# Optimization experiments

Hardware: AMD Instinct MI355X
Metric: run time of the kernel (lower is better)

Reference implementation:

```python
import jax, jax.numpy as jnp
import numpy as np

LAMBDA_MIN = 0.1
LAMBDA_GLOBAL_MIN = 0.1
LAMBDA_GLOBAL_SCALE = 1.0
SLOPE = 0.2  # negative_slope


def leaky(x):
    return jnp.where(x >= 0, x, SLOPE * x)


def setup_inputs() -> dict:
    key = jax.random.key(0)
    ks = jax.random.split(key, 16)
    n, d, E, C, R = 10000, 128, 320000, 50000, 20
    s = 0.05
    h = jax.random.normal(ks[0], (n, d), jnp.float32)
    edge_index = jax.random.randint(ks[1], (2, E), 0, n)
    edge_type = jax.random.randint(ks[2], (E,), 0, R)
    rel_table = jax.random.normal(ks[3], (R, d), jnp.float32) * s
    # constraints taken from a subset of edges so matches exist
    constraint_indices = edge_index[:, :C]
    constraint_values = jax.random.normal(ks[4], (C,), jnp.float32)
    constraint_types = jax.random.randint(ks[5], (C,), 0, 4)
    att_in = 3 * d  # out*2 + in_dim (use_relation)
    W = jax.random.normal(ks[6], (d, d), jnp.float32) * s
    W_bi = jax.random.normal(ks[7], (d, d), jnp.float32) * s
    att_w1 = jax.random.normal(ks[8], (d, att_in), jnp.float32) * s
    att_b1 = jnp.zeros((d,), jnp.float32)
    att_w2 = jax.random.normal(ks[9], (d,), jnp.float32) * s
    gate_w1 = jax.random.normal(ks[10], (d, 2 * d), jnp.float32) * s
    gate_b1 = jnp.zeros((d,), jnp.float32)
    gate_w2 = jax.random.normal(ks[11], (d,), jnp.float32) * s
    gate_b2 = jnp.zeros((), jnp.float32)
    lambda_c = jnp.full((4,), 0.5, jnp.float32)  # CONSTRAINT_LAMBDA_INIT
    lambda_global = jnp.array(0.5, jnp.float32)
    return dict(h=h, edge_index=edge_index, edge_type=edge_type,
                rel_table=rel_table, constraint_indices=constraint_indices,
                constraint_values=constraint_values, constraint_types=constraint_types,
                W=W, W_bi=W_bi, att_w1=att_w1, att_b1=att_b1, att_w2=att_w2,
                gate_w1=gate_w1, gate_b1=gate_b1, gate_w2=gate_w2, gate_b2=gate_b2,
                lambda_c=lambda_c, lambda_global=lambda_global)


def reference(h, edge_index, edge_type, rel_table, constraint_indices,
              constraint_values, constraint_types, W, W_bi, att_w1, att_b1,
              att_w2, gate_w1, gate_b1, gate_w2, gate_b2, lambda_c, lambda_global):
    n = h.shape[0]
    Wh = h @ W.T                                  # [n, d]
    src, tgt = edge_index[0], edge_index[1]
    src_emb, tgt_emb = Wh[src], Wh[tgt]           # [E, d]
    r_emb = rel_table[edge_type]                  # [E, d]
    att_in = jnp.concatenate([src_emb, tgt_emb, r_emb], axis=-1)  # [E, 3d]
    e = leaky(att_in @ att_w1.T + att_b1) @ att_w2                # [E]

    # ---- constraints (bounded lambdas) ----
    lc = jax.nn.sigmoid(lambda_c) * (1.0 - LAMBDA_MIN) + LAMBDA_MIN
    lg = jax.nn.sigmoid(lambda_global) * (LAMBDA_GLOBAL_SCALE - LAMBDA_GLOBAL_MIN) + LAMBDA_GLOBAL_MIN
    ws = lc[constraint_types] * constraint_values                 # [C]
    c_keys = constraint_indices[0] * n + constraint_indices[1]
    e_keys = src * n + tgt
    # O(n^2) scatter buffers, faithful to the original
    c_agg = jnp.zeros((n * n,), jnp.float32).at[c_keys].add(ws)
    c_exists = jnp.zeros((n * n,), jnp.float32).at[c_keys].add(1.0)
    ms = c_agg[e_keys]
    mask = c_exists[e_keys] > 0
    ms = ms * mask.astype(jnp.float32)
    # constraint gate on matched edges (unmatched entries are 0 anyway)
    gi = jnp.concatenate([src_emb, tgt_emb], axis=-1)             # [E, 2d]
    g = jax.nn.sigmoid(leaky(gi @ gate_w1.T + gate_b1) @ gate_w2 + gate_b2)
    ms = jnp.where(mask, g * ms, ms)
    n_matched = mask.sum()
    global_bias = lg * jnp.mean(ws) * 0.01
    e = jnp.where(n_matched > 0, e + lg * ms, e + global_bias)

    # ---- scatter softmax over src neighborhoods ----
    mx = jax.ops.segment_max(e, src, num_segments=n)
    ex = jnp.exp(jnp.minimum(e - mx[src], 20.0))
    sm = jax.ops.segment_sum(ex, src, num_segments=n)
    attn = ex / (sm[src] + 1e-10)                                 # [E]

    # ---- weighted scatter-add aggregation ----
    side = jax.ops.segment_sum(attn[:, None] * tgt_emb, src, num_segments=n)  # [n, d]

    sum_out = leaky(Wh + side)
    bi_out = leaky((Wh * side) @ W_bi.T)
    h_new = sum_out + bi_out + Wh   # bi-interaction + residual
    return jax.nn.elu(h_new)
```

## Files before the change

### kernel.cpp

```cpp
#include <hip/hip_runtime.h>
#include <stdint.h>

#define SLOPE 0.2f
#define HASH_SIZE 131072
#define POIS ((int)0xAAAAAAAA)
#define MAXDEG 64

typedef __attribute__((ext_vector_type(8))) short bf16x8;
typedef __attribute__((ext_vector_type(4))) float f32x4;

__device__ __forceinline__ float leakyf(float x) { return fmaxf(x, SLOPE * x); }
__device__ __forceinline__ float sigmoidf(float x) { return 1.f / (1.f + __expf(-x)); }
__device__ __forceinline__ unsigned short f2bf(float f) {
  union { float f; unsigned int i; } c; c.f = f;
  unsigned int u = c.i;
  return (unsigned short)((u + 0x7fffu + ((u >> 16) & 1u)) >> 16);
}
__device__ __forceinline__ void unpk8(uint4 v, float* o) {
  union { unsigned int i; float f; } t;
  t.i = v.x << 16;          o[0] = t.f;
  t.i = v.x & 0xffff0000u;  o[1] = t.f;
  t.i = v.y << 16;          o[2] = t.f;
  t.i = v.y & 0xffff0000u;  o[3] = t.f;
  t.i = v.z << 16;          o[4] = t.f;
  t.i = v.z & 0xffff0000u;  o[5] = t.f;
  t.i = v.w << 16;          o[6] = t.f;
  t.i = v.w & 0xffff0000u;  o[7] = t.f;
}
__device__ __forceinline__ void ldbf8(const unsigned short* p, float* o) {
  unpk8(*(const uint4*)p, o);
}

__device__ __forceinline__ void mfma_core_a(const bf16x8 (&afr)[4],
                                            const unsigned short* bptr, f32x4 (&acc)[8]) {
  #pragma unroll
  for (int ks = 0; ks < 4; ++ks) {
    #pragma unroll
    for (int ct = 0; ct < 8; ++ct) {
      bf16x8 b = *(const bf16x8*)(bptr + ct * 2048 + ks * 32);
      acc[ct] = __builtin_amdgcn_mfma_f32_16x16x32_bf16(afr[ks], b, acc[ct], 0, 0, 0);
    }
  }
}

__global__ __launch_bounds__(256) void setup_kernel(
    const float* __restrict__ aw1, const float* __restrict__ gw1,
    const float* __restrict__ W, const float* __restrict__ Wbi,
    const float* __restrict__ rel, const float* __restrict__ ab1,
    const int* __restrict__ cidx, const float* __restrict__ cval,
    const int* __restrict__ ctype, const float* __restrict__ lc,
    unsigned short* __restrict__ Wcat, unsigned short* __restrict__ P3b16,
    int* __restrict__ hkeys,
    int C, int n, int R, int H)
{
  int i0 = blockIdx.x * blockDim.x + threadIdx.x;
  int stride = gridDim.x * blockDim.x;
  for (int j = i0; j < 6 * 16384; j += stride) {
    int mat = j >> 14, rest = j & 16383, col = rest >> 7, k = rest & 127;
    float v;
    switch (mat) {
      case 0:  v = aw1[col * 384 + k]; break;
      case 1:  v = aw1[col * 384 + 128 + k]; break;
      case 2:  v = gw1[col * 256 + k]; break;
      case 3:  v = gw1[col * 256 + 128 + k]; break;
      case 4:  v = W[col * 128 + k]; break;
      default: v = Wbi[col * 128 + k]; break;
    }
    Wcat[j] = f2bf(v);
  }
  for (int it = i0; it < R * 128; it += stride) {
    int r = it >> 7, jj = it & 127;
    float acc = ab1[jj];
    const float4* wrow = (const float4*)(aw1 + jj * 384 + 256);
    const float4* rl   = (const float4*)(rel + r * 128);
    #pragma unroll 8
    for (int k = 0; k < 32; ++k) {
      float4 a = rl[k], b = wrow[k];
      acc += a.x * b.x + a.y * b.y + a.z * b.z + a.w * b.w;
    }
    P3b16[it] = f2bf(acc);
  }
  for (int j = i0; j < C; j += stride) {
    int key = cidx[j] * n + cidx[C + j];
    float l = sigmoidf(lc[ctype[j]]) * 0.9f + 0.1f;
    float w = l * cval[j];
    unsigned int slot = ((unsigned int)key * 2654435761u) & (unsigned int)(H - 1);
    while (true) {
      int prev = atomicCAS(&hkeys[2 * slot], POIS, key);
      if (prev == POIS || prev == key) break;
      slot = (slot + 1) & (unsigned int)(H - 1);
    }
    atomicAdd((float*)&hkeys[2 * slot + 1], w);
  }
}

__device__ __forceinline__ void store_tile(const unsigned short (*t)[136],
                                           unsigned short* __restrict__ out,
                                           int rs, int rows_left, int lane)
{
  const int c = (lane & 15) * 8, q = lane >> 4;
  #pragma unroll
  for (int ro = 0; ro < 4; ++ro) {
    int row = ro * 4 + q;
    bf16x8 v = *(const bf16x8*)&t[row][c];
    if (row < rows_left)
      *(bf16x8*)(out + row * rs + c) = v;
  }
}

__global__ __launch_bounds__(256) void gemm_place(
    const int* __restrict__ ei, const int* __restrict__ etype,
    int* __restrict__ cursor2, int2* __restrict__ trs2, int E,
    const float* __restrict__ h, const unsigned short* __restrict__ Wcat,
    const int2* __restrict__ hk,
    unsigned short* __restrict__ PW, unsigned short* __restrict__ PQ,
    unsigned short* __restrict__ Q2b,
    int n, int NB5, int H)
{
  if ((int)blockIdx.x >= NB5) {
    int i = ((int)blockIdx.x - NB5) * 256 + threadIdx.x;
    if (i < E) {
      int s = ei[i], t = ei[E + i], rt = etype[i];
      float ms = 0.f;
      bool found = false;
      int key = s * n + t;
      unsigned int slot = ((unsigned int)key * 2654435761u) & (unsigned int)(H - 1);
      while (true) {
        int2 kv = hk[slot];
        if (kv.x == key) { ms = __int_as_float(kv.y); found = true; break; }
        if (kv.x == POIS) break;
        slot = (slot + 1) & (unsigned int)(H - 1);
      }
      int rec = t | (rt << 14);
      if (found) {
        int k = atomicAdd(&cursor2[2 * s], 1) - POIS;
        if (k < MAXDEG)
          trs2[(size_t)s * MAXDEG + k] = make_int2(rec, __float_as_int(ms));
      } else {
        int k = atomicAdd(&cursor2[2 * s + 1], 1) - POIS;
        int bp = MAXDEG - 1 - k;
        if (bp >= 0)
          trs2[(size_t)s * MAXDEG + bp] = make_int2(rec, 0);
      }
    }
    return;
  }
  __shared__ unsigned short tile[4][16][136];
  const int wv = (int)threadIdx.x >> 6, lane = (int)threadIdx.x & 63;
  const int m0 = ((int)blockIdx.x * 4 + wv) * 16;
  if (m0 >= n) return;
  const int r = lane & 15, quad = lane >> 4;
  const int rows_left = n - m0;

  bf16x8 afr[4];
  const float* hrow = h + (size_t)min(m0 + r, n - 1) * 128 + quad * 8;
  #pragma unroll
  for (int ks = 0; ks < 4; ++ks) {
    float4 f0 = *(const float4*)(hrow + ks * 32);
    float4 f1 = *(const float4*)(hrow + ks * 32 + 4);
    bf16x8 a;
    a[0] = (short)f2bf(f0.x); a[1] = (short)f2bf(f0.y);
    a[2] = (short)f2bf(f0.z); a[3] = (short)f2bf(f0.w);
    a[4] = (short)f2bf(f1.x); a[5] = (short)f2bf(f1.y);
    a[6] = (short)f2bf(f1.z); a[7] = (short)f2bf(f1.w);
    afr[ks] = a;
  }

  f32x4 acc[8] = {};
  mfma_core_a(afr, Wcat + 4 * 16384 + r * 128 + quad * 8, acc);
  #pragma unroll
  for (int ct = 0; ct < 8; ++ct)
    #pragma unroll
    for (int rg = 0; rg < 4; ++rg)
      tile[wv][quad * 4 + rg][ct * 16 + r] = f2bf(acc[ct][rg]);

  bf16x8 wfr[4];
  #pragma unroll
  for (int ks = 0; ks < 4; ++ks)
    wfr[ks] = *(const bf16x8*)&tile[wv][r][quad * 8 + ks * 32];

  store_tile(tile[wv], PW + (size_t)m0 * 256 + 128, 256, rows_left, lane);

  #pragma unroll
  for (int mat = 0; mat < 4; ++mat) {
    f32x4 a2[8] = {};
    mfma_core_a(wfr, Wcat + mat * 16384 + r * 128 + quad * 8, a2);
    #pragma unroll
    for (int ct = 0; ct < 8; ++ct)
      #pragma unroll
      for (int rg = 0; rg < 4; ++rg)
        tile[wv][quad * 4 + rg][ct * 16 + r] = f2bf(a2[ct][rg]);
    unsigned short* out; int rs;
    if (mat == 0)      { out = PQ  + (size_t)m0 * 256;        rs = 256; }
    else if (mat == 1) { out = PW  + (size_t)m0 * 256;        rs = 256; }
    else if (mat == 2) { out = PQ  + (size_t)m0 * 256 + 128;  rs = 256; }
    else               { out = Q2b + (size_t)m0 * 128;        rs = 128; }
    store_tile(tile[wv], out, rs, rows_left, lane);
  }
}

__global__ __launch_bounds__(256) void fused_node_final(
  const int* __restrict__ cursor2,
  const int2* __restrict__ trs2,
  const unsigned short* __restrict__ PQ, const unsigned short* __restrict__ PW,
  const unsigned short* __restrict__ P3b16, const unsigned short* __restrict__ Q2,
  const float* __restrict__ aw2, const float* __restrict__ gb1,
  const float* __restrict__ gw2, const float* __restrict__ gb2,
  const float* __restrict__ lgp,
  const unsigned short* __restrict__ Wcat5,
  float* __restrict__ outp, int n, int R)
{
  __shared__ unsigned short P3l[20 * 128];
  __shared__ unsigned short Xt[4][136];
  __shared__ float          Ft[4][132];

  for (int j = threadIdx.x; j < R * 64; j += 256)
    ((unsigned int*)P3l)[j] = ((const unsigned int*)P3b16)[j];
  __syncthreads();

  const int wv = (int)threadIdx.x >> 6;
  const int lane = (int)threadIdx.x & 63;
  const int g = lane >> 4;
  const int u = lane & 15;
  const int d0 = u * 8;

  const int node = (int)blockIdx.x * 4 + wv;
  const bool anode = node < n;

  if (anode) {
    const int2 cc2 = *(const int2*)&cursor2[2 * node];
    const int cM = min(cc2.x - POIS, MAXDEG);
    const int cU = min(cc2.y - POIS, MAXDEG - cM);
    const int2 ment = trs2[(size_t)node * MAXDEG + lane];

    float p1v[8], w2v[8], qbv[8], g2v[8];
    const unsigned short* pqrow = PQ + (size_t)node * 256 + d0;
    ldbf8(pqrow, p1v);
    { float q1t[8]; ldbf8(pqrow + 128, q1t);
      float4 bA = *(const float4*)(gb1 + d0), bB = *(const float4*)(gb1 + d0 + 4);
      qbv[0]=q1t[0]+bA.x; qbv[1]=q1t[1]+bA.y; qbv[2]=q1t[2]+bA.z; qbv[3]=q1t[3]+bA.w;
      qbv[4]=q1t[4]+bB.x; qbv[5]=q1t[5]+bB.y; qbv[6]=q1t[6]+bB.z; qbv[7]=q1t[7]+bB.w; }
    { float4 a = *(const float4*)(aw2 + d0), b = *(const float4*)(aw2 + d0 + 4);
      w2v[0]=a.x; w2v[1]=a.y; w2v[2]=a.z; w2v[3]=a.w;
      w2v[4]=b.x; w2v[5]=b.y; w2v[6]=b.z; w2v[7]=b.w; }
    { float4 a = *(const float4*)(gw2 + d0), b = *(const float4*)(gw2 + d0 + 4);
      g2v[0]=a.x; g2v[1]=a.y; g2v[2]=a.z; g2v[3]=a.w;
      g2v[4]=b.x; g2v[5]=b.y; g2v[6]=b.z; g2v[7]=b.w; }
    float gb2s = gb2[0];
    float lg = sigmoidf(lgp[0]) * 0.9f + 0.1f;

    float sg = 0.f;
    float acc[8] = {};

    const int itM = (cM + 3) >> 2;
    const int itU = (cU + 3) >> 2;

    struct StageU { uint4 rpa, rwv; int rt; bool act; };

    auto issueU = [&](int j) -> StageU {
      StageU st;
      int jj = min(j, cU - 1);
      int bp = MAXDEG - cU + jj;
      int bx = __shfl(ment.x, bp, 64);
      int tx = bx & 16383;
      st.rt = (bx >> 14) & 31;
      const unsigned short* pw = PW + (size_t)tx * 256 + d0;
      st.rpa = *(const uint4*)pw;
      st.rwv = *(const uint4*)(pw + 128);
      st.act = j < cU;
      return st;
    };

    auto consumeU = [&](const StageU& st) {
      float pa[8], cc[8];
      unpk8(st.rpa, pa);
      ldbf8(&P3l[st.rt * 128 + d0], cc);
      float s = 0.f;
      #pragma unroll
      for (int d = 0; d < 8; ++d) s += leakyf(p1v[d] + pa[d] + cc[d]) * w2v[d];
      #pragma unroll
      for (int d = 1; d < 16; d <<= 1) s += __shfl_xor(s, d, 64);
      if (st.act) {
        float wvv[8];
        unpk8(st.rwv, wvv);
        float p = __expf(s);
        sg += p;
        #pragma unroll
        for (int d = 0; d < 8; ++d) acc[d] += p * wvv[d];
      }
    };

    StageU A, B;
    if (itU > 0) A = issueU(g);

    for (int i = 0; i < itM; ++i) {
      int e = i * 4 + g;
      int idx = min(e, cM - 1);
      int bx = __shfl(ment.x, idx, 64);
      int by = __shfl(ment.y, idx, 64);
      int tx = bx & 16383, rt = (bx >> 14) & 31;
      const unsigned short* pw = PW + (size_t)tx * 256 + d0;
      uint4 rpa = *(const uint4*)pw;
      uint4 rwv = *(const uint4*)(pw + 128);
      uint4 rcc = *(const uint4*)&P3l[rt * 128 + d0];
      uint4 rq2 = *(const uint4*)(Q2 + (size_t)tx * 128 + d0);
      float ms = __int_as_float(by);

      float pa[8], cc[8];
      unpk8(rpa, pa);
      unpk8(rcc, cc);
      float s = 0.f;
      #pragma unroll
      for (int d = 0; d < 8; ++d) s += leakyf(p1v[d] + pa[d] + cc[d]) * w2v[d];
      #pragma unroll
      for (int d = 1; d < 16; d <<= 1) s += __shfl_xor(s, d, 64);

      float q2[8];
      unpk8(rq2, q2);
      float gp = 0.f;
      #pragma unroll
      for (int d = 0; d < 8; ++d) gp += leakyf(qbv[d] + q2[d]) * g2v[d];
      #pragma unroll
      for (int d = 1; d < 16; d <<= 1) gp += __shfl_xor(gp, d, 64);
      s += lg * (sigmoidf(gp + gb2s) * ms);

      if (e < cM) {
        float wvv[8];
        unpk8(rwv, wvv);
        float p = __expf(s);
        sg += p;
        #pragma unroll
        for (int d = 0; d < 8; ++d) acc[d] += p * wvv[d];
      }
    }

    if (itU > 1) B = issueU(4 + g);
    for (int i = 0; i < itU; ++i) {
      StageU Cst;
      if (i + 2 < itU) Cst = issueU((i + 2) * 4 + g);
      consumeU(A);
      A = B; B = Cst;
    }

    sg += __shfl_xor(sg, 16, 64);
    sg += __shfl_xor(sg, 32, 64);
    #pragma unroll
    for (int d = 0; d < 8; ++d) {
      acc[d] += __shfl_xor(acc[d], 16, 64);
      acc[d] += __shfl_xor(acc[d], 32, 64);
    }

    if (g == 0) {
      float inv = 1.f / (sg + 1e-10f);
      float wh[8];
      ldbf8(PW + (size_t)node * 256 + 128 + d0, wh);
      bf16x8 xv;
      float fv[8];
      #pragma unroll
      for (int d = 0; d < 8; ++d) {
        float sd = acc[d] * inv;
        xv[d] = (short)f2bf(wh[d] * sd);
        fv[d] = leakyf(wh[d] + sd) + wh[d];
      }
      *(bf16x8*)&Xt[wv][d0] = xv;
      *(f32x4*)&Ft[wv][d0]     = *(const f32x4*)&fv[0];
      *(f32x4*)&Ft[wv][d0 + 4] = *(const f32x4*)&fv[4];
    }
  }
  __syncthreads();

  bf16x8 afr2[4];
  #pragma unroll
  for (int ks = 0; ks < 4; ++ks)
    afr2[ks] = *(const bf16x8*)&Xt[u & 3][g * 8 + ks * 32];
  f32x4 ac0 = {}, ac1 = {};
  const unsigned short* bb = Wcat5 + (size_t)(wv * 2) * 2048 + u * 128 + g * 8;
  #pragma unroll
  for (int ks = 0; ks < 4; ++ks) {
    bf16x8 b0 = *(const bf16x8*)(bb + ks * 32);
    bf16x8 b1 = *(const bf16x8*)(bb + 2048 + ks * 32);
    ac0 = __builtin_amdgcn_mfma_f32_16x16x32_bf16(afr2[ks], b0, ac0, 0, 0, 0);
    ac1 = __builtin_amdgcn_mfma_f32_16x16x32_bf16(afr2[ks], b1, ac1, 0, 0, 0);
  }
  if (g == 0) {
    const int base = (int)blockIdx.x * 4;
    const int c0 = wv * 32 + u, c1 = c0 + 16;
    #pragma unroll
    for (int rg = 0; rg < 4; ++rg) {
      int nrow = base + rg;
      if (nrow < n) {
        float hn0 = Ft[rg][c0] + leakyf(ac0[rg]);
        float hn1 = Ft[rg][c1] + leakyf(ac1[rg]);
        outp[(size_t)nrow * 128 + c0] = hn0 > 0.f ? hn0 : __expf(hn0) - 1.f;
        outp[(size_t)nrow * 128 + c1] = hn1 > 0.f ? hn1 : __expf(hn1) - 1.f;
      }
    }
  }
}

extern "C" void kernel_launch(void* const* d_in, const int* in_sizes, int n_in,
                              void* d_out, int out_size, void* d_ws, size_t ws_size,
                              hipStream_t stream)
{
  const float* h    = (const float*)d_in[0];
  const int* ei     = (const int*)d_in[1];
  const int* etype  = (const int*)d_in[2];
  const float* rel  = (const float*)d_in[3];
  const int* cidx   = (const int*)d_in[4];
  const float* cval = (const float*)d_in[5];
  const int* ctype  = (const int*)d_in[6];
  const float* W    = (const float*)d_in[7];
  const float* Wbi  = (const float*)d_in[8];
  const float* aw1  = (const float*)d_in[9];
  const float* ab1  = (const float*)d_in[10];
  const float* aw2  = (const float*)d_in[11];
  const float* gw1  = (const float*)d_in[12];
  const float* gb1  = (const float*)d_in[13];
  const float* gw2  = (const float*)d_in[14];
  const float* gb2  = (const float*)d_in[15];
  const float* lc   = (const float*)d_in[16];
  const float* lgp  = (const float*)d_in[17];

  const int n = in_sizes[0] / 128;
  const int E = in_sizes[2];
  const int C = in_sizes[6];
  const int R = in_sizes[3] / 128;
  const int H = HASH_SIZE;

  char* ws = (char*)d_ws;
  size_t off = 0;
  auto alloc = [&](size_t bytes) -> void* {
    void* p = ws + off;
    off = (off + bytes + 255) & ~(size_t)255;
    return p;
  };
  unsigned short* PW    = (unsigned short*)alloc((size_t)n * 256 * 2);
  unsigned short* PQ    = (unsigned short*)alloc((size_t)n * 256 * 2);
  unsigned short* Q2b   = (unsigned short*)alloc((size_t)n * 128 * 2);
  unsigned short* Wcat  = (unsigned short*)alloc((size_t)6 * 128 * 128 * 2);
  unsigned short* P3b16 = (unsigned short*)alloc((size_t)R * 128 * 2);
  int2* trs2   = (int2*)alloc((size_t)n * MAXDEG * 8);
  int* cursor2 = (int*)alloc((size_t)n * 8);
  int* hki     = (int*)alloc((size_t)H * 8);
  (void)ws_size; (void)n_in; (void)out_size;

  const int NB5 = (n + 63) / 64;
  const int NBP = (E + 255) / 256;
  const int NB4 = (n + 3) / 4;

  setup_kernel<<<512, 256, 0, stream>>>(aw1, gw1, W, Wbi, rel, ab1,
                                        cidx, cval, ctype, lc,
                                        Wcat, P3b16, hki, C, n, R, H);
  gemm_place<<<NB5 + NBP, 256, 0, stream>>>(ei, etype, cursor2, trs2, E,
                                            h, Wcat, (const int2*)hki,
                                            PW, PQ, Q2b, n, NB5, H);
  fused_node_final<<<NB4, 256, 0, stream>>>(cursor2, trs2, PQ, PW, P3b16, Q2b,
                                            aw2, gb1, gw2, gb2, lgp,
                                            Wcat + 5 * 16384, (float*)d_out, n, R);
}
```

Baseline: 177.6 us.

## Prefetch unmatched-edge rows into LDS with async global_load_lds triple buffering

The unmatched-edge loop used to prefetch neighbour PW rows into registers through a two-stage software pipeline. It now issues `global_load_lds` direct-to-LDS copies into a per-wave triple buffer and waits with explicit `s_waitcnt vmcnt(2)` before reading the current slot. The aim is to free registers and keep more gather loads in flight to hide memory latency. The cost is about 24 KB of extra LDS per block, which may reduce occupancy. Correctness now relies on hand-placed vmcnt accounting, and a few redundant clamped loads are issued past the end of the loop.

```diff
diff --git a/kernel.cpp b/kernel.cpp
--- a/kernel.cpp
+++ b/kernel.cpp
@@ -8,6 +8,10 @@
 
 typedef __attribute__((ext_vector_type(8))) short bf16x8;
 typedef __attribute__((ext_vector_type(4))) float f32x4;
+
+#define GLOAD_LDS16(gp, lp) __builtin_amdgcn_global_load_lds(                 \
+    (const __attribute__((address_space(1))) void*)(gp),                      \
+    (__attribute__((address_space(3))) void*)(lp), 16, 0, 0)
 
 __device__ __forceinline__ float leakyf(float x) { return fmaxf(x, SLOPE * x); }
 __device__ __forceinline__ float sigmoidf(float x) { return 1.f / (1.f + __expf(-x)); }
@@ -211,6 +215,7 @@
   float* __restrict__ outp, int n, int R)
 {
   __shared__ unsigned short P3l[20 * 128];
+  __shared__ unsigned short Gst[4][3][2][4][16][8];
   __shared__ unsigned short Xt[4][136];
   __shared__ float          Ft[4][132];
 
@@ -255,43 +260,17 @@
     const int itM = (cM + 3) >> 2;
     const int itU = (cU + 3) >> 2;
 
-    struct StageU { uint4 rpa, rwv; int rt; bool act; };
-
-    auto issueU = [&](int j) -> StageU {
-      StageU st;
-      int jj = min(j, cU - 1);
-      int bp = MAXDEG - cU + jj;
+    auto issueL = [&](int i, int slot) {
+      int e = min(i * 4 + g, cU - 1);
+      int bp = MAXDEG - cU + e;
       int bx = __shfl(ment.x, bp, 64);
       int tx = bx & 16383;
-      st.rt = (bx >> 14) & 31;
-      const unsigned short* pw = PW + (size_t)tx * 256 + d0;
-      st.rpa = *(const uint4*)pw;
-      st.rwv = *(const uint4*)(pw + 128);
-      st.act = j < cU;
-      return st;
+      const unsigned short* pw = PW + (size_t)tx * 256 + u * 8;
+      GLOAD_LDS16(pw,       &Gst[wv][slot][0][0][0][0]);
+      GLOAD_LDS16(pw + 128, &Gst[wv][slot][1][0][0][0]);
     };
 
-    auto consumeU = [&](const StageU& st) {
-      float pa[8], cc[8];
-      unpk8(st.rpa, pa);
-      ldbf8(&P3l[st.rt * 128 + d0], cc);
-      float s = 0.f;
-      #pragma unroll
-      for (int d = 0; d < 8; ++d) s += leakyf(p1v[d] + pa[d] + cc[d]) * w2v[d];
-      #pragma unroll
-      for (int d = 1; d < 16; d <<= 1) s += __shfl_xor(s, d, 64);
-      if (st.act) {
-        float wvv[8];
-        unpk8(st.rwv, wvv);
-        float p = __expf(s);
-        sg += p;
-        #pragma unroll
-        for (int d = 0; d < 8; ++d) acc[d] += p * wvv[d];
-      }
-    };
-
-    StageU A, B;
-    if (itU > 0) A = issueU(g);
+    if (itU > 0) { issueL(0, 0); issueL(1, 1); }
 
     for (int i = 0; i < itM; ++i) {
       int e = i * 4 + g;
@@ -334,12 +313,33 @@
       }
     }
 
-    if (itU > 1) B = issueU(4 + g);
     for (int i = 0; i < itU; ++i) {
-      StageU Cst;
-      if (i + 2 < itU) Cst = issueU((i + 2) * 4 + g);
-      consumeU(A);
-      A = B; B = Cst;
+      const int slot = i % 3;
+      asm volatile("s_waitcnt vmcnt(2)" ::: "memory");
+      int e0 = i * 4 + g;
+      int e = min(e0, cU - 1);
+      int bp = MAXDEG - cU + e;
+      int bx = __shfl(ment.x, bp, 64);
+      int rt = (bx >> 14) & 31;
+      uint4 rpa = *(const uint4*)&Gst[wv][slot][0][g][u][0];
+      uint4 rwv = *(const uint4*)&Gst[wv][slot][1][g][u][0];
+      float pa[8], cc[8];
+      unpk8(rpa, pa);
+      ldbf8(&P3l[rt * 128 + d0], cc);
+      float s = 0.f;
+      #pragma unroll
+      for (int d = 0; d < 8; ++d) s += leakyf(p1v[d] + pa[d] + cc[d]) * w2v[d];
+      #pragma unroll
+      for (int d = 1; d < 16; d <<= 1) s += __shfl_xor(s, d, 64);
+      if (e0 < cU) {
+        float wvv[8];
+        unpk8(rwv, wvv);
+        float p = __expf(s);
+        sg += p;
+        #pragma unroll
+        for (int d = 0; d < 8; ++d) acc[d] += p * wvv[d];
+      }
+      issueL(i + 2, (i + 2) % 3);
     }
 
     sg += __shfl_xor(sg, 16, 64);
```

New measurement: 178.6 us. About the same (+0.5%).
